# Performance work log

Hardware: AMD Instinct MI355X
Metric: run time of the kernel (lower is better)

The kernel has to match this reference:

```python
import jax, jax.numpy as jnp
import numpy as np

def binarize(t):
    # deterministic sign binarization to {-1, +1}
    return jnp.where(t >= 0, 1.0, -1.0).astype(t.dtype)

def setup_inputs() -> dict:
    key = jax.random.key(0)
    k1, k2 = jax.random.split(key)
    x = jax.random.normal(k1, (8192, 4096), dtype=jnp.float32)
    kernel = jax.random.normal(k2, (4096, 4096), dtype=jnp.float32)
    return {"x": x, "kernel": kernel}

def reference(x, kernel):
    # BinaryLayer.call with binary=True: matmul(binarize(x), binarize(W))
    return jnp.matmul(binarize(x), binarize(kernel))
```

## Files before the change

kernel.cpp:

```cpp
#include <hip/hip_runtime.h>
#include <stdint.h>

#define MDIM 8192
#define NDIM 4096
#define KDIM 4096
#define KB2  (KDIM / 2)
#define BKB  128
#define NKT  (KDIM / 256)

#define BM 256
#define BN 256
#define ABUF      32768
#define BUFSTRIDE 65536

typedef __attribute__((ext_vector_type(4))) int   i32x4;
typedef __attribute__((ext_vector_type(8))) int   i32x8;
typedef __attribute__((ext_vector_type(4))) float f32x4;

__device__ __forceinline__ void gload16(const void* g, void* l) {
    __builtin_amdgcn_global_load_lds(
        (const __attribute__((address_space(1))) void*)g,
        (__attribute__((address_space(3))) void*)l, 16, 0, 0);
}

__device__ __forceinline__ i32x8 pad8(i32x4 v) {
    i32x8 r;
    r[0] = v[0]; r[1] = v[1]; r[2] = v[2]; r[3] = v[3];
    r[4] = 0;    r[5] = 0;    r[6] = 0;    r[7] = 0;
    return r;
}

#define MFMA_FP4(a, b, c)                                                   \
    __builtin_amdgcn_mfma_scale_f32_16x16x128_f8f6f4(                        \
        (a), (b), (c), 4, 4, 0, 0x7F7F7F7F, 0, 0x7F7F7F7F)

__global__ __launch_bounds__(256) void pack_a4_kernel(const float* __restrict__ X,
                                                      uint8_t* __restrict__ A4) {
    size_t gt = (size_t)blockIdx.x * 256 + threadIdx.x;
    const float4* x4 = (const float4*)X + gt * 4;
    uint32_t out[2] = {0, 0};
#pragma unroll
    for (int q = 0; q < 4; ++q) {
        float4 v = x4[q];
        uint32_t b0 = (v.x >= 0.f ? 0x2u : 0xAu) | ((v.y >= 0.f ? 0x2u : 0xAu) << 4);
        uint32_t b1 = (v.z >= 0.f ? 0x2u : 0xAu) | ((v.w >= 0.f ? 0x2u : 0xAu) << 4);
        out[q >> 1] |= (b0 | (b1 << 8)) << ((q & 1) * 16);
    }
    ((uint2*)A4)[gt] = make_uint2(out[0], out[1]);
}

__global__ __launch_bounds__(256) void pack_b4t_kernel(const float* __restrict__ W,
                                                       uint8_t* __restrict__ B4) {
    __shared__ uint8_t t[64][72];
    const int tid = threadIdx.x;
    const int k0 = blockIdx.y * 64, n0 = blockIdx.x * 64;
#pragma unroll
    for (int r = 0; r < 4; ++r) {
        int e  = r * 1024 + tid * 4;
        int k  = e >> 6;
        int nn = e & 63;
        float4 v = *(const float4*)&W[(size_t)(k0 + k) * NDIM + n0 + nn];
        uint32_t b0 = (v.x >= 0.f) ? 0x2u : 0xAu;
        uint32_t b1 = (v.y >= 0.f) ? 0x2u : 0xAu;
        uint32_t b2 = (v.z >= 0.f) ? 0x2u : 0xAu;
        uint32_t b3 = (v.w >= 0.f) ? 0x2u : 0xAu;
        *(uint32_t*)&t[k][nn] = b0 | (b1 << 8) | (b2 << 16) | (b3 << 24);
    }
    __syncthreads();
    const int n = tid >> 2, kc = tid & 3;
    uint32_t w[2] = {0, 0};
#pragma unroll
    for (int b = 0; b < 8; ++b) {
        int k = kc * 16 + b * 2;
        uint32_t byte = (uint32_t)t[k][n] | ((uint32_t)t[k + 1][n] << 4);
        w[b >> 2] |= byte << ((b & 3) * 8);
    }
    *(uint2*)&B4[(size_t)(n0 + n) * KB2 + k0 / 2 + kc * 8] = make_uint2(w[0], w[1]);
}

__global__ __launch_bounds__(512, 2) void binmm_fp4_kernel(const uint8_t* __restrict__ A4,
                                                           const uint8_t* __restrict__ B4,
                                                           float* __restrict__ C) {
    __shared__ uint8_t lds[2 * BUFSTRIDE];

    const int tid = threadIdx.x, lane = tid & 63, wid = tid >> 6;
    const int wr = wid >> 2, wc = wid & 3;
    const int l15 = lane & 15, g = (lane >> 4) & 3;
    const int m0 = blockIdx.y * BM, n0 = blockIdx.x * BN;

    const int srow  = tid >> 3;
    const int sslot = tid & 7;
    const uint8_t* gA[4];
    const uint8_t* gB[4];
#pragma unroll
    for (int p = 0; p < 4; ++p) {
        int row = srow + p * 64;
        int ss  = (sslot ^ (row & 7)) * 16;
        gA[p] = A4 + (size_t)(m0 + row) * KB2 + ss;
        gB[p] = B4 + (size_t)(n0 + row) * KB2 + ss;
    }

    f32x4 acc[8][4];
#pragma unroll
    for (int m = 0; m < 8; ++m)
#pragma unroll
        for (int n = 0; n < 4; ++n) acc[m][n] = (f32x4){0.f, 0.f, 0.f, 0.f};

    auto stageA = [&](int nxt) {
#pragma unroll
        for (int p = 0; p < 4; ++p) {
            gload16(gA[p], lds + nxt + tid * 16 + p * 8192);
            gA[p] += BKB;
        }
    };
    auto stageB = [&](int nxt) {
#pragma unroll
        for (int p = 0; p < 4; ++p) {
            gload16(gB[p], lds + nxt + ABUF + tid * 16 + p * 8192);
            gB[p] += BKB;
        }
    };

#define RD_A(dst, buf, s, half) do {                                           \
        _Pragma("unroll")                                                      \
        for (int mf = 0; mf < 4; ++mf) {                                       \
            int row = wr * 128 + (half) * 64 + mf * 16 + l15;                  \
            dst[mf] = *(const i32x4*)(lds + (buf) + row * 128 +                \
                                      ((((s) * 4 + g) ^ (row & 7)) * 16));     \
        }                                                                      \
    } while (0)
#define RD_B(dst, buf, s) do {                                                 \
        _Pragma("unroll")                                                      \
        for (int nf = 0; nf < 4; ++nf) {                                       \
            int row = wc * 64 + nf * 16 + l15;                                 \
            dst[nf] = *(const i32x4*)(lds + (buf) + ABUF + row * 128 +         \
                                      ((((s) * 4 + g) ^ (row & 7)) * 16));     \
        }                                                                      \
    } while (0)
#define CLUSTER(AS, BS, half) do {                                             \
        __builtin_amdgcn_s_setprio(1);                                         \
        _Pragma("unroll")                                                      \
        for (int mf = 0; mf < 4; ++mf) {                                       \
            i32x8 a8 = pad8(AS[mf]);                                           \
            acc[(half) * 4 + mf][0] = MFMA_FP4(a8, pad8(BS[0]), acc[(half) * 4 + mf][0]); \
            acc[(half) * 4 + mf][1] = MFMA_FP4(a8, pad8(BS[1]), acc[(half) * 4 + mf][1]); \
            acc[(half) * 4 + mf][2] = MFMA_FP4(a8, pad8(BS[2]), acc[(half) * 4 + mf][2]); \
            acc[(half) * 4 + mf][3] = MFMA_FP4(a8, pad8(BS[3]), acc[(half) * 4 + mf][3]); \
        }                                                                      \
        __builtin_amdgcn_s_setprio(0);                                         \
    } while (0)

    i32x4 aC[4], aN[4], bC[4], bN[4];

    auto tile = [&](int cur, int nxt, bool do_stage, bool rd_next) {
        RD_A(aN, cur, 0, 1);
        if (do_stage) stageA(nxt);
        CLUSTER(aC, bC, 0);
        RD_B(bN, cur, 1);
        RD_A(aC, cur, 1, 0);
        if (do_stage) stageB(nxt);
        CLUSTER(aN, bC, 1);
        RD_A(aN, cur, 1, 1);
        CLUSTER(aC, bN, 0);
        CLUSTER(aN, bN, 1);
        __syncthreads();
        if (rd_next) {
            RD_B(bC, nxt, 0);
            RD_A(aC, nxt, 0, 0);
        }
    };

    stageA(0); stageB(0);
    __syncthreads();
    RD_B(bC, 0, 0);
    RD_A(aC, 0, 0, 0);

#pragma unroll 1
    for (int tt = 0; tt < NKT / 2 - 1; ++tt) {
        tile(0, BUFSTRIDE, true, true);
        tile(BUFSTRIDE, 0, true, true);
    }
    tile(0, BUFSTRIDE, true, true);
    tile(BUFSTRIDE, 0, false, false);

#pragma unroll
    for (int mf = 0; mf < 8; ++mf) {
#pragma unroll
        for (int nf = 0; nf < 4; ++nf) {
            size_t cc = (size_t)(n0 + wc * 64 + nf * 16 + l15);
            int rbase = m0 + wr * 128 + mf * 16 + g * 4;
#pragma unroll
            for (int reg = 0; reg < 4; ++reg)
                C[(size_t)(rbase + reg) * NDIM + cc] = acc[mf][nf][reg];
        }
    }
}

extern "C" void kernel_launch(void* const* d_in, const int* in_sizes, int n_in,
                              void* d_out, int out_size, void* d_ws, size_t ws_size,
                              hipStream_t stream) {
    const float* x = (const float*)d_in[0];
    const float* w = (const float*)d_in[1];
    float* out = (float*)d_out;

    uint8_t* A4 = (uint8_t*)d_ws;
    uint8_t* B4 = (uint8_t*)d_ws + (size_t)MDIM * KB2;

    pack_a4_kernel<<<(int)((size_t)MDIM * KDIM / 16 / 256), 256, 0, stream>>>(x, A4);
    pack_b4t_kernel<<<dim3(NDIM / 64, KDIM / 64), 256, 0, stream>>>(w, B4);
    binmm_fp4_kernel<<<dim3(NDIM / BN, MDIM / BM), 512, 0, stream>>>(A4, B4, out);
}
```

Baseline: 124.7 us.

## Switch to 4-stage LDS ring with smaller K tiles and vmcnt-based waits

Halves the per-stage K tile to 128 elements (64 bytes) and replaces the double-buffered 64KB scheme with a 4-deep ring of 32KB buffers. Loads are kept three stages ahead, and each barrier waits with explicit s_waitcnt vmcnt counts instead of a full drain. The LDS swizzle changes to match 64-byte rows, and the compute step interleaves A-fragment reads with the MFMAs. The aim is deeper global-load latency hiding at the cost of twice as many barriers per K and shorter compute bursts between them.

```diff
diff --git a/kernel.cpp b/kernel.cpp
--- a/kernel.cpp
+++ b/kernel.cpp
@@ -5,13 +5,12 @@
 #define NDIM 4096
 #define KDIM 4096
 #define KB2  (KDIM / 2)
-#define BKB  128
-#define NKT  (KDIM / 256)
+#define BKB  64
+#define NT   (KDIM / 128)
 
 #define BM 256
 #define BN 256
-#define ABUF      32768
-#define BUFSTRIDE 65536
+#define BUFSZ 32768
 
 typedef __attribute__((ext_vector_type(4))) int   i32x4;
 typedef __attribute__((ext_vector_type(8))) int   i32x8;
@@ -81,24 +80,32 @@
 __global__ __launch_bounds__(512, 2) void binmm_fp4_kernel(const uint8_t* __restrict__ A4,
                                                            const uint8_t* __restrict__ B4,
                                                            float* __restrict__ C) {
-    __shared__ uint8_t lds[2 * BUFSTRIDE];
+    __shared__ uint8_t lds[4 * BUFSZ];
 
     const int tid = threadIdx.x, lane = tid & 63, wid = tid >> 6;
     const int wr = wid >> 2, wc = wid & 3;
     const int l15 = lane & 15, g = (lane >> 4) & 3;
     const int m0 = blockIdx.y * BM, n0 = blockIdx.x * BN;
 
-    const int srow  = tid >> 3;
-    const int sslot = tid & 7;
-    const uint8_t* gA[4];
-    const uint8_t* gB[4];
-#pragma unroll
-    for (int p = 0; p < 4; ++p) {
-        int row = srow + p * 64;
-        int ss  = (sslot ^ (row & 7)) * 16;
-        gA[p] = A4 + (size_t)(m0 + row) * KB2 + ss;
-        gB[p] = B4 + (size_t)(n0 + row) * KB2 + ss;
-    }
+    const int srowp = tid >> 2;
+    const int fS    = (tid >> 3) & 3;
+    const int csrc  = ((tid & 3) ^ fS) * 16;
+    const uint8_t* pA0 = A4 + (size_t)(m0 + srowp)       * KB2 + csrc;
+    const uint8_t* pA1 = A4 + (size_t)(m0 + 128 + srowp) * KB2 + csrc;
+    const uint8_t* pB0 = B4 + (size_t)(n0 + srowp)       * KB2 + csrc;
+    const uint8_t* pB1 = B4 + (size_t)(n0 + 128 + srowp) * KB2 + csrc;
+
+#define STAGE(bufOff) do {                                                     \
+        gload16(pA0, lds + (bufOff) + tid * 16);                               \
+        gload16(pA1, lds + (bufOff) + 8192  + tid * 16);                       \
+        gload16(pB0, lds + (bufOff) + 16384 + tid * 16);                       \
+        gload16(pB1, lds + (bufOff) + 24576 + tid * 16);                       \
+        pA0 += BKB; pA1 += BKB; pB0 += BKB; pB1 += BKB;                        \
+    } while (0)
+
+    const int fR = (l15 >> 1) & 3;
+    const int aBase = (wr * 128 + l15) * 64 + ((g ^ fR) * 16);
+    const int bBase = 16384 + (wc * 64 + l15) * 64 + ((g ^ fR) * 16);
 
     f32x4 acc[8][4];
 #pragma unroll
@@ -106,82 +113,49 @@
 #pragma unroll
         for (int n = 0; n < 4; ++n) acc[m][n] = (f32x4){0.f, 0.f, 0.f, 0.f};
 
-    auto stageA = [&](int nxt) {
-#pragma unroll
-        for (int p = 0; p < 4; ++p) {
-            gload16(gA[p], lds + nxt + tid * 16 + p * 8192);
-            gA[p] += BKB;
-        }
-    };
-    auto stageB = [&](int nxt) {
-#pragma unroll
-        for (int p = 0; p < 4; ++p) {
-            gload16(gB[p], lds + nxt + ABUF + tid * 16 + p * 8192);
-            gB[p] += BKB;
-        }
-    };
-
-#define RD_A(dst, buf, s, half) do {                                           \
-        _Pragma("unroll")                                                      \
-        for (int mf = 0; mf < 4; ++mf) {                                       \
-            int row = wr * 128 + (half) * 64 + mf * 16 + l15;                  \
-            dst[mf] = *(const i32x4*)(lds + (buf) + row * 128 +                \
-                                      ((((s) * 4 + g) ^ (row & 7)) * 16));     \
-        }                                                                      \
-    } while (0)
-#define RD_B(dst, buf, s) do {                                                 \
-        _Pragma("unroll")                                                      \
-        for (int nf = 0; nf < 4; ++nf) {                                       \
-            int row = wc * 64 + nf * 16 + l15;                                 \
-            dst[nf] = *(const i32x4*)(lds + (buf) + ABUF + row * 128 +         \
-                                      ((((s) * 4 + g) ^ (row & 7)) * 16));     \
-        }                                                                      \
-    } while (0)
-#define CLUSTER(AS, BS, half) do {                                             \
+#define COMPUTE(bufOff) do {                                                   \
+        const uint8_t* bp_ = lds + (bufOff);                                   \
+        i32x8 b8_0 = pad8(*(const i32x4*)(bp_ + bBase));                       \
+        i32x8 b8_1 = pad8(*(const i32x4*)(bp_ + bBase + 1024));                \
+        i32x8 b8_2 = pad8(*(const i32x4*)(bp_ + bBase + 2048));                \
+        i32x8 b8_3 = pad8(*(const i32x4*)(bp_ + bBase + 3072));                \
+        i32x4 aN = *(const i32x4*)(bp_ + aBase);                               \
         __builtin_amdgcn_s_setprio(1);                                         \
         _Pragma("unroll")                                                      \
-        for (int mf = 0; mf < 4; ++mf) {                                       \
-            i32x8 a8 = pad8(AS[mf]);                                           \
-            acc[(half) * 4 + mf][0] = MFMA_FP4(a8, pad8(BS[0]), acc[(half) * 4 + mf][0]); \
-            acc[(half) * 4 + mf][1] = MFMA_FP4(a8, pad8(BS[1]), acc[(half) * 4 + mf][1]); \
-            acc[(half) * 4 + mf][2] = MFMA_FP4(a8, pad8(BS[2]), acc[(half) * 4 + mf][2]); \
-            acc[(half) * 4 + mf][3] = MFMA_FP4(a8, pad8(BS[3]), acc[(half) * 4 + mf][3]); \
+        for (int mf = 0; mf < 8; ++mf) {                                       \
+            i32x8 a8 = pad8(aN);                                               \
+            if (mf < 7) aN = *(const i32x4*)(bp_ + aBase + (mf + 1) * 1024);   \
+            acc[mf][0] = MFMA_FP4(a8, b8_0, acc[mf][0]);                       \
+            acc[mf][1] = MFMA_FP4(a8, b8_1, acc[mf][1]);                       \
+            acc[mf][2] = MFMA_FP4(a8, b8_2, acc[mf][2]);                       \
+            acc[mf][3] = MFMA_FP4(a8, b8_3, acc[mf][3]);                       \
         }                                                                      \
         __builtin_amdgcn_s_setprio(0);                                         \
     } while (0)
 
-    i32x4 aC[4], aN[4], bC[4], bN[4];
+#define SYNC(n) do {                                                           \
+        __builtin_amdgcn_sched_barrier(0);                                     \
+        asm volatile("s_waitcnt vmcnt(" #n ")" ::: "memory");                  \
+        __builtin_amdgcn_s_barrier();                                          \
+        __builtin_amdgcn_sched_barrier(0);                                     \
+    } while (0)
 
-    auto tile = [&](int cur, int nxt, bool do_stage, bool rd_next) {
-        RD_A(aN, cur, 0, 1);
-        if (do_stage) stageA(nxt);
-        CLUSTER(aC, bC, 0);
-        RD_B(bN, cur, 1);
-        RD_A(aC, cur, 1, 0);
-        if (do_stage) stageB(nxt);
-        CLUSTER(aN, bC, 1);
-        RD_A(aN, cur, 1, 1);
-        CLUSTER(aC, bN, 0);
-        CLUSTER(aN, bN, 1);
-        __syncthreads();
-        if (rd_next) {
-            RD_B(bC, nxt, 0);
-            RD_A(aC, nxt, 0, 0);
-        }
-    };
-
-    stageA(0); stageB(0);
-    __syncthreads();
-    RD_B(bC, 0, 0);
-    RD_A(aC, 0, 0, 0);
+    STAGE(0);
+    STAGE(BUFSZ);
+    STAGE(2 * BUFSZ);
+    SYNC(8);
 
 #pragma unroll 1
-    for (int tt = 0; tt < NKT / 2 - 1; ++tt) {
-        tile(0, BUFSTRIDE, true, true);
-        tile(BUFSTRIDE, 0, true, true);
+    for (int t = 0; t < NT - 3; ++t) {
+        STAGE(((t + 3) & 3) * BUFSZ);
+        COMPUTE((t & 3) * BUFSZ);
+        SYNC(8);
     }
-    tile(0, BUFSTRIDE, true, true);
-    tile(BUFSTRIDE, 0, false, false);
+    COMPUTE(1 * BUFSZ);
+    SYNC(4);
+    COMPUTE(2 * BUFSZ);
+    SYNC(0);
+    COMPUTE(3 * BUFSZ);
 
 #pragma unroll
     for (int mf = 0; mf < 8; ++mf) {
@@ -194,6 +168,9 @@
                 C[(size_t)(rbase + reg) * NDIM + cc] = acc[mf][nf][reg];
         }
     }
+#undef STAGE
+#undef COMPUTE
+#undef SYNC
 }
 
 extern "C" void kernel_launch(void* const* d_in, const int* in_sizes, int n_in,
```

Result: no change. 126.0 us (+1.1%).
